# Kernel tuning notes

Hardware: AMD Instinct MI355X
Metric: run time of the kernel (lower is better)

The kernel has to match this reference:

```python
import jax, jax.numpy as jnp
import numpy as np

B, K, I, H, LAT = 128, 32, 12000, 600, 200
TAU = 0.1
EPS = 1e-12  # torch F.normalize eps


def _l2norm(x):
    return x / jnp.maximum(jnp.linalg.norm(x, axis=-1, keepdims=True), EPS)


def _l1norm(x):
    return x / jnp.maximum(jnp.sum(jnp.abs(x), axis=-1, keepdims=True), EPS)


def setup_inputs() -> dict:
    key = jax.random.key(0)
    ks = jax.random.split(key, 8)
    rating_matrix = jax.random.normal(ks[0], (B, I), dtype=jnp.float32)
    items_idx = jax.random.randint(ks[1], (B, K), 0, I)
    gram_matrix = jax.random.normal(ks[2], (I, I), dtype=jnp.float32)
    # xavier-ish scaling so tanh / exp stay in a sane range
    W1 = jax.random.normal(ks[3], (I, H), dtype=jnp.float32) * (1.0 / np.sqrt(I))
    b1 = jax.random.normal(ks[4], (H,), dtype=jnp.float32) * 0.001
    W2 = jax.random.normal(ks[5], (H, 2 * LAT), dtype=jnp.float32) * (1.0 / np.sqrt(H))
    b2 = jax.random.normal(ks[6], (2 * LAT,), dtype=jnp.float32) * 0.001
    items = jax.random.normal(ks[7], (I, LAT), dtype=jnp.float32)
    return {"rating_matrix": rating_matrix, "items_idx": items_idx,
            "gram_matrix": gram_matrix, "W1": W1, "b1": b1,
            "W2": W2, "b2": b2, "items": items}


def reference(rating_matrix, items_idx, gram_matrix, W1, b1, W2, b2, items):
    # eval-mode forward_kernel_1226 with a fixed K interacted items per user
    b0 = _l2norm(rating_matrix)                       # [B, I]
    u = (b0 > 0).astype(rating_matrix.dtype)          # binary user row [B, I]
    g = gram_matrix[items_idx]                        # gather: [B, K, I]
    x = _l2norm(_l1norm(g * u[:, None, :]))           # mask + L1 + L2 normalize
    h = jnp.tanh(jnp.einsum('bki,ih->bkh', x, W1) + b1)
    enc = jnp.einsum('bkh,ho->bko', h, W2) + b2       # [B, K, 2*LAT]
    mean, logvar = jnp.split(enc, 2, axis=-1)
    z = mean                                          # eval: z = mean
    out = jnp.einsum('bkd,id->bki', _l2norm(z), _l2norm(items)) / TAU
    # equal-length segmented mean-exp-log reduce over the K rows per user
    new_output = jnp.log(jnp.mean(jnp.exp(out), axis=1) + 1.0)  # [B, I]
    kl = 0.5 * jnp.mean(jnp.sum(mean ** 2 + jnp.exp(logvar) - 1.0 - logvar, axis=-1))
    return z.reshape(B * K, LAT), new_output, kl, x.reshape(B * K, I)
```

## Files before the change

kernel.cpp:

```cpp
#include <hip/hip_runtime.h>

typedef unsigned short u16;
typedef __attribute__((ext_vector_type(8))) short bf16x8;
typedef __attribute__((ext_vector_type(4))) float f32x4;

#define MFMA16x16(a, b, c) __builtin_amdgcn_mfma_f32_16x16x32_bf16((a), (b), (c), 0, 0, 0)

#define N_B 128
#define N_K 32
#define N_I 12000
#define N_H 600
#define N_HP 640
#define N_LAT 200
#define N_DP 224
#define N_2LAT 400
#define N_ROWS 4096
#define EPSF 1e-12f

#define OFF_NO 819200
#define OFF_KL 2355200
#define OFF_X  2355201

__device__ __forceinline__ u16 f2bf(float f) {
    unsigned u = __builtin_bit_cast(unsigned, f);
    return (u16)((u + 0x7fffu + ((u >> 16) & 1u)) >> 16);
}

__global__ __launch_bounds__(256) void k_w1t(const float* __restrict__ W1, u16* __restrict__ w1t) {
    __shared__ float tile[32][33];
    const int k0 = blockIdx.x * 32, n0 = blockIdx.y * 32;
    const int x = threadIdx.x, y = threadIdx.y;
#pragma unroll
    for (int r = 0; r < 4; r++) {
        int kk = y * 4 + r;
        int n = n0 + x;
        tile[kk][x] = (n < N_H) ? W1[(size_t)(k0 + kk) * N_H + n] : 0.f;
    }
    __syncthreads();
#pragma unroll
    for (int r = 0; r < 4; r++) {
        int nl = y * 4 + r;
        w1t[(size_t)(n0 + nl) * N_I + k0 + x] = f2bf(tile[x][nl]);
    }
}

__global__ __launch_bounds__(256) void k_w2t(const float* __restrict__ W2, u16* __restrict__ w2t) {
    __shared__ float tile[32][33];
    const int k0 = blockIdx.x * 32, n0 = blockIdx.y * 32;
    const int x = threadIdx.x, y = threadIdx.y;
#pragma unroll
    for (int r = 0; r < 4; r++) {
        int kk = y * 4 + r;
        int n = n0 + x;
        tile[kk][x] = ((k0 + kk) < N_H && n < N_2LAT) ? W2[(size_t)(k0 + kk) * N_2LAT + n] : 0.f;
    }
    __syncthreads();
#pragma unroll
    for (int r = 0; r < 4; r++) {
        int nl = y * 4 + r;
        if (n0 + nl < N_2LAT)
            w2t[(size_t)(n0 + nl) * N_HP + k0 + x] = f2bf(tile[x][nl]);
    }
}

__global__ __launch_bounds__(256) void k_itemn(const float* __restrict__ items, u16* __restrict__ itn) {
    const int r = blockIdx.x * 4 + (threadIdx.x >> 6);
    const int lane = threadIdx.x & 63;
    const float4* src = (const float4*)(items + (size_t)r * N_LAT);
    float4 v = make_float4(0.f, 0.f, 0.f, 0.f);
    if (lane < 50) v = src[lane];
    float sq = v.x * v.x + v.y * v.y + v.z * v.z + v.w * v.w;
#pragma unroll
    for (int m = 1; m < 64; m <<= 1) sq += __shfl_xor(sq, m);
    const float inv = 1.f / fmaxf(sqrtf(sq), EPSF);
    u16* dst = itn + (size_t)r * N_DP;
    if (lane < 50) {
        ushort4 pk;
        pk.x = f2bf(v.x * inv); pk.y = f2bf(v.y * inv);
        pk.z = f2bf(v.z * inv); pk.w = f2bf(v.w * inv);
        *(ushort4*)(dst + lane * 4) = pk;
    } else if (lane < 56) {
        ushort4 pk; pk.x = 0; pk.y = 0; pk.z = 0; pk.w = 0;
        *(ushort4*)(dst + lane * 4) = pk;
    }
}

__global__ __launch_bounds__(256) void k_xnorm(const float* __restrict__ rating, const int* __restrict__ idx,
                                               const float* __restrict__ gram, float* __restrict__ x_out,
                                               u16* __restrict__ xb) {
    const int row = blockIdx.x;
    const int b = row >> 5;
    const int gi = idx[row];
    const float4* grow = (const float4*)(gram + (size_t)gi * N_I);
    const float4* urow = (const float4*)(rating + (size_t)b * N_I);
    float sa = 0.f, sq = 0.f;
    for (int i = threadIdx.x; i < N_I / 4; i += 256) {
        float4 g = grow[i], u = urow[i];
        float m0 = u.x > 0.f ? g.x : 0.f;
        float m1 = u.y > 0.f ? g.y : 0.f;
        float m2 = u.z > 0.f ? g.z : 0.f;
        float m3 = u.w > 0.f ? g.w : 0.f;
        sa += fabsf(m0) + fabsf(m1) + fabsf(m2) + fabsf(m3);
        sq += m0 * m0 + m1 * m1 + m2 * m2 + m3 * m3;
    }
    __shared__ float red[8];
#pragma unroll
    for (int m = 1; m < 64; m <<= 1) { sa += __shfl_xor(sa, m); sq += __shfl_xor(sq, m); }
    const int w = threadIdx.x >> 6;
    if ((threadIdx.x & 63) == 0) { red[w] = sa; red[4 + w] = sq; }
    __syncthreads();
    sa = red[0] + red[1] + red[2] + red[3];
    sq = red[4] + red[5] + red[6] + red[7];
    const float s1 = fmaxf(sa, EPSF);
    const float s2 = fmaxf(sqrtf(sq) / s1, EPSF);
    const float scale = 1.f / (s1 * s2);
    float* xo = x_out + (size_t)row * N_I;
    u16* xbo = xb + (size_t)row * N_I;
    for (int i = threadIdx.x; i < N_I / 4; i += 256) {
        float4 g = grow[i], u = urow[i];
        float m0 = (u.x > 0.f ? g.x : 0.f) * scale;
        float m1 = (u.y > 0.f ? g.y : 0.f) * scale;
        float m2 = (u.z > 0.f ? g.z : 0.f) * scale;
        float m3 = (u.w > 0.f ? g.w : 0.f) * scale;
        xo[i * 4 + 0] = m0; xo[i * 4 + 1] = m1; xo[i * 4 + 2] = m2; xo[i * 4 + 3] = m3;
        ushort4 pk;
        pk.x = f2bf(m0); pk.y = f2bf(m1); pk.z = f2bf(m2); pk.w = f2bf(m3);
        *(ushort4*)(xbo + i * 4) = pk;
    }
}

__global__ __launch_bounds__(256) void k_gemm1(const u16* __restrict__ xb, const u16* __restrict__ w1t,
                                               const float* __restrict__ b1, u16* __restrict__ hbuf) {
    __shared__ u16 Als[128 * 40];
    __shared__ u16 Bls[128 * 40];
    const int m0 = blockIdx.x * 128;
    const int n0 = blockIdx.y * 128;
    const int t = threadIdx.x;
    const int lane = t & 63, w = t >> 6;
    const int wr = (w >> 1) * 64, wc = (w & 1) * 64;
    const int q = lane >> 4, l15 = lane & 15;

    const int rA0 = t >> 2, cA = t & 3;
    const int rA1 = rA0 + 64;
    const size_t xg0 = (size_t)(m0 + rA0) * N_I + cA * 8;
    const size_t xg1 = (size_t)(m0 + rA1) * N_I + cA * 8;
    const size_t wg0 = (size_t)(n0 + rA0) * N_I + cA * 8;
    const size_t wg1 = (size_t)(n0 + rA1) * N_I + cA * 8;
    const int ls0 = rA0 * 40 + cA * 8;
    const int ls1 = rA1 * 40 + cA * 8;

    f32x4 acc[4][4];
#pragma unroll
    for (int i = 0; i < 4; i++)
#pragma unroll
        for (int j = 0; j < 4; j++) acc[i][j] = (f32x4){0.f, 0.f, 0.f, 0.f};

    for (int k0 = 0; k0 < N_I; k0 += 32) {
        uint4 a0 = *(const uint4*)(xb + xg0 + k0);
        uint4 a1 = *(const uint4*)(xb + xg1 + k0);
        uint4 g0 = *(const uint4*)(w1t + wg0 + k0);
        uint4 g1 = *(const uint4*)(w1t + wg1 + k0);
        __syncthreads();
        *(uint4*)(Als + ls0) = a0;
        *(uint4*)(Als + ls1) = a1;
        *(uint4*)(Bls + ls0) = g0;
        *(uint4*)(Bls + ls1) = g1;
        __syncthreads();
        bf16x8 af[4], bf[4];
#pragma unroll
        for (int f = 0; f < 4; f++) af[f] = *(const bf16x8*)(Als + (wr + f * 16 + l15) * 40 + q * 8);
#pragma unroll
        for (int f = 0; f < 4; f++) bf[f] = *(const bf16x8*)(Bls + (wc + f * 16 + l15) * 40 + q * 8);
#pragma unroll
        for (int fm = 0; fm < 4; fm++)
#pragma unroll
            for (int fn = 0; fn < 4; fn++)
                acc[fm][fn] = MFMA16x16(af[fm], bf[fn], acc[fm][fn]);
    }
#pragma unroll
    for (int fm = 0; fm < 4; fm++) {
        const int rowb = m0 + wr + fm * 16 + q * 4;
#pragma unroll
        for (int fn = 0; fn < 4; fn++) {
            const int col = n0 + wc + fn * 16 + l15;
            const float bias = (col < N_H) ? b1[col] : 0.f;
#pragma unroll
            for (int r = 0; r < 4; r++) {
                float e = acc[fm][fn][r] + bias;
                hbuf[(size_t)(rowb + r) * N_HP + col] = f2bf(tanhf(e));
            }
        }
    }
}

__global__ __launch_bounds__(64) void k_gemm2(const u16* __restrict__ hbuf, const u16* __restrict__ w2t,
                                              const float* __restrict__ b2, float* __restrict__ z_out,
                                              float* __restrict__ kl_out, u16* __restrict__ znb) {
    const int m0 = blockIdx.x * 16;
    const int lane = threadIdx.x;
    const int q = lane >> 4, l15 = lane & 15;
    f32x4 acc[25];
#pragma unroll
    for (int f = 0; f < 25; f++) acc[f] = (f32x4){0.f, 0.f, 0.f, 0.f};
    for (int s = 0; s < N_HP / 32; s++) {
        bf16x8 a = *(const bf16x8*)(hbuf + (size_t)(m0 + l15) * N_HP + s * 32 + q * 8);
#pragma unroll
        for (int f = 0; f < 25; f++) {
            bf16x8 bb = *(const bf16x8*)(w2t + (size_t)(f * 16 + l15) * N_HP + s * 32 + q * 8);
            acc[f] = MFMA16x16(a, bb, acc[f]);
        }
    }
    float sumsq[4] = {0.f, 0.f, 0.f, 0.f}, kls[4] = {0.f, 0.f, 0.f, 0.f};
#pragma unroll
    for (int f = 0; f < 25; f++) {
        const int n = f * 16 + l15;
        const float bias = b2[n];
#pragma unroll
        for (int r = 0; r < 4; r++) {
            float e = acc[f][r] + bias;
            if (n < N_LAT) {
                sumsq[r] += e * e;
                kls[r] += e * e;
                z_out[(size_t)(m0 + q * 4 + r) * N_LAT + n] = e;
            } else {
                kls[r] += __expf(e) - 1.f - e;
            }
        }
    }
#pragma unroll
    for (int r = 0; r < 4; r++)
#pragma unroll
        for (int m = 1; m < 16; m <<= 1) {
            sumsq[r] += __shfl_xor(sumsq[r], m);
            kls[r] += __shfl_xor(kls[r], m);
        }
    float inv[4];
#pragma unroll
    for (int r = 0; r < 4; r++) inv[r] = 1.f / fmaxf(sqrtf(sumsq[r]), EPSF);
#pragma unroll
    for (int f = 0; f < 25; f++) {
        const int n = f * 16 + l15;
        const float bias = b2[n];
#pragma unroll
        for (int r = 0; r < 4; r++) {
            const int row = m0 + q * 4 + r;
            float e = acc[f][r] + bias;
            if (n < N_LAT) znb[(size_t)row * N_DP + n] = f2bf(e * inv[r]);
            else if (n < N_DP) znb[(size_t)row * N_DP + n] = 0;
        }
    }
    if (l15 == 0) {
        float s = (kls[0] + kls[1] + kls[2] + kls[3]) * (0.5f / (float)N_ROWS);
        atomicAdd(kl_out, s);
    }
}

__global__ __launch_bounds__(256) void k_outred(const u16* __restrict__ znb, const u16* __restrict__ itn,
                                                float* __restrict__ no_out) {
    __shared__ u16 zls[32 * N_DP];
    const int b = blockIdx.x;
    const int t = threadIdx.x;
    for (int i = t; i < (32 * N_DP) / 8; i += 256)
        ((uint4*)zls)[i] = ((const uint4*)(znb + (size_t)b * 32 * N_DP))[i];
    __syncthreads();
    const int lane = t & 63, w = t >> 6;
    const int q = lane >> 4, l15 = lane & 15;
    bf16x8 af[2][7];
#pragma unroll
    for (int hh = 0; hh < 2; hh++)
#pragma unroll
        for (int s = 0; s < 7; s++)
            af[hh][s] = *(const bf16x8*)(zls + (hh * 16 + l15) * N_DP + s * 32 + q * 8);
    for (int tt = blockIdx.y * 4 + w; tt < 750; tt += 128) {
        const int i0 = tt * 16;
        bf16x8 bfr[7];
#pragma unroll
        for (int s = 0; s < 7; s++)
            bfr[s] = *(const bf16x8*)(itn + (size_t)(i0 + l15) * N_DP + s * 32 + q * 8);
        f32x4 a0 = (f32x4){0.f, 0.f, 0.f, 0.f}, a1 = (f32x4){0.f, 0.f, 0.f, 0.f};
#pragma unroll
        for (int s = 0; s < 7; s++) {
            a0 = MFMA16x16(af[0][s], bfr[s], a0);
            a1 = MFMA16x16(af[1][s], bfr[s], a1);
        }
        float se = 0.f;
#pragma unroll
        for (int r = 0; r < 4; r++) se += __expf(a0[r] * 10.f) + __expf(a1[r] * 10.f);
        se += __shfl_xor(se, 16);
        se += __shfl_xor(se, 32);
        if (lane < 16)
            no_out[(size_t)b * N_I + i0 + lane] = __logf(se * (1.f / 32.f) + 1.f);
    }
}

extern "C" void kernel_launch(void* const* d_in, const int* in_sizes, int n_in,
                              void* d_out, int out_size, void* d_ws, size_t ws_size,
                              hipStream_t stream) {
    const float* rating = (const float*)d_in[0];
    const int* idx = (const int*)d_in[1];
    const float* gram = (const float*)d_in[2];
    const float* W1 = (const float*)d_in[3];
    const float* b1 = (const float*)d_in[4];
    const float* W2 = (const float*)d_in[5];
    const float* b2 = (const float*)d_in[6];
    const float* items = (const float*)d_in[7];

    float* out = (float*)d_out;
    float* z_out = out;
    float* no_out = out + OFF_NO;
    float* kl_out = out + OFF_KL;
    float* x_out = out + OFF_X;

    char* ws = (char*)d_ws;
    u16* xb   = (u16*)(ws);
    u16* w1t  = (u16*)(ws + 98304000);
    u16* w2t  = (u16*)(ws + 113664000);
    u16* hbuf = (u16*)(ws + 114176000);
    u16* znb  = (u16*)(ws + 119418880);
    u16* itn  = (u16*)(ws + 121253888);

    hipMemsetAsync(kl_out, 0, 4, stream);
    k_w1t<<<dim3(N_I / 32, N_HP / 32), dim3(32, 8), 0, stream>>>(W1, w1t);
    k_w2t<<<dim3(N_HP / 32, 13), dim3(32, 8), 0, stream>>>(W2, w2t);
    k_itemn<<<N_I / 4, 256, 0, stream>>>(items, itn);
    k_xnorm<<<N_ROWS, 256, 0, stream>>>(rating, idx, gram, x_out, xb);
    k_gemm1<<<dim3(N_ROWS / 128, N_HP / 128), 256, 0, stream>>>(xb, w1t, b1, hbuf);
    k_gemm2<<<N_ROWS / 16, 64, 0, stream>>>(hbuf, w2t, b2, z_out, kl_out, znb);
    k_outred<<<dim3(N_B, 32), 256, 0, stream>>>(znb, itn, no_out);
}
```

Before: 1.289 ms.

## Split-K gemm1 with async LDS loads, register-cached xnorm, two-user outred

The first GEMM is split along K into five chunks. Each chunk loads its tiles with direct global-to-LDS async loads and accumulates partial sums into a zeroed fp32 buffer using atomics. A separate kernel then adds the bias and applies an exp-based tanh. The base grid had only 32x5 blocks, and the split raises that parallelism at the cost of atomic traffic and an extra pass. k_xnorm now keeps the masked row in registers so gram is not read twice, k_outred handles two users per block so each item tile load is reused, and the workspace is reorganised so hbuf aliases xb.

```diff
diff --git a/kernel.cpp b/kernel.cpp
--- a/kernel.cpp
+++ b/kernel.cpp
@@ -16,6 +16,8 @@
 #define N_2LAT 400
 #define N_ROWS 4096
 #define EPSF 1e-12f
+#define SPLITK 5
+#define KC 2400
 
 #define OFF_NO 819200
 #define OFF_KL 2355200
@@ -24,6 +26,12 @@
 __device__ __forceinline__ u16 f2bf(float f) {
     unsigned u = __builtin_bit_cast(unsigned, f);
     return (u16)((u + 0x7fffu + ((u >> 16) & 1u)) >> 16);
+}
+
+__device__ __forceinline__ void async_ld16(const u16* g, u16* l) {
+    __builtin_amdgcn_global_load_lds(
+        (const __attribute__((address_space(1))) unsigned int*)g,
+        (__attribute__((address_space(3))) unsigned int*)l, 16, 0, 0);
 }
 
 __global__ __launch_bounds__(256) void k_w1t(const float* __restrict__ W1, u16* __restrict__ w1t) {
@@ -93,15 +101,22 @@
     const int gi = idx[row];
     const float4* grow = (const float4*)(gram + (size_t)gi * N_I);
     const float4* urow = (const float4*)(rating + (size_t)b * N_I);
+    float4 mv[12];
     float sa = 0.f, sq = 0.f;
-    for (int i = threadIdx.x; i < N_I / 4; i += 256) {
-        float4 g = grow[i], u = urow[i];
-        float m0 = u.x > 0.f ? g.x : 0.f;
-        float m1 = u.y > 0.f ? g.y : 0.f;
-        float m2 = u.z > 0.f ? g.z : 0.f;
-        float m3 = u.w > 0.f ? g.w : 0.f;
-        sa += fabsf(m0) + fabsf(m1) + fabsf(m2) + fabsf(m3);
-        sq += m0 * m0 + m1 * m1 + m2 * m2 + m3 * m3;
+#pragma unroll
+    for (int j = 0; j < 12; j++) {
+        int i = threadIdx.x + j * 256;
+        if (i < N_I / 4) {
+            float4 g = grow[i], u = urow[i];
+            float4 m;
+            m.x = u.x > 0.f ? g.x : 0.f;
+            m.y = u.y > 0.f ? g.y : 0.f;
+            m.z = u.z > 0.f ? g.z : 0.f;
+            m.w = u.w > 0.f ? g.w : 0.f;
+            mv[j] = m;
+            sa += fabsf(m.x) + fabsf(m.y) + fabsf(m.z) + fabsf(m.w);
+            sq += m.x * m.x + m.y * m.y + m.z * m.z + m.w * m.w;
+        }
     }
     __shared__ float red[8];
 #pragma unroll
@@ -116,38 +131,42 @@
     const float scale = 1.f / (s1 * s2);
     float* xo = x_out + (size_t)row * N_I;
     u16* xbo = xb + (size_t)row * N_I;
-    for (int i = threadIdx.x; i < N_I / 4; i += 256) {
-        float4 g = grow[i], u = urow[i];
-        float m0 = (u.x > 0.f ? g.x : 0.f) * scale;
-        float m1 = (u.y > 0.f ? g.y : 0.f) * scale;
-        float m2 = (u.z > 0.f ? g.z : 0.f) * scale;
-        float m3 = (u.w > 0.f ? g.w : 0.f) * scale;
-        xo[i * 4 + 0] = m0; xo[i * 4 + 1] = m1; xo[i * 4 + 2] = m2; xo[i * 4 + 3] = m3;
-        ushort4 pk;
-        pk.x = f2bf(m0); pk.y = f2bf(m1); pk.z = f2bf(m2); pk.w = f2bf(m3);
-        *(ushort4*)(xbo + i * 4) = pk;
+#pragma unroll
+    for (int j = 0; j < 12; j++) {
+        int i = threadIdx.x + j * 256;
+        if (i < N_I / 4) {
+            float4 m = mv[j];
+            float m0 = m.x * scale, m1 = m.y * scale, m2 = m.z * scale, m3 = m.w * scale;
+            xo[i * 4 + 0] = m0; xo[i * 4 + 1] = m1; xo[i * 4 + 2] = m2; xo[i * 4 + 3] = m3;
+            ushort4 pk;
+            pk.x = f2bf(m0); pk.y = f2bf(m1); pk.z = f2bf(m2); pk.w = f2bf(m3);
+            *(ushort4*)(xbo + i * 4) = pk;
+        }
     }
 }
 
 __global__ __launch_bounds__(256) void k_gemm1(const u16* __restrict__ xb, const u16* __restrict__ w1t,
-                                               const float* __restrict__ b1, u16* __restrict__ hbuf) {
-    __shared__ u16 Als[128 * 40];
-    __shared__ u16 Bls[128 * 40];
+                                               float* __restrict__ accbuf) {
+    __shared__ u16 Als[128 * 32];
+    __shared__ u16 Bls[128 * 32];
     const int m0 = blockIdx.x * 128;
     const int n0 = blockIdx.y * 128;
+    const int kbase = blockIdx.z * KC;
     const int t = threadIdx.x;
     const int lane = t & 63, w = t >> 6;
     const int wr = (w >> 1) * 64, wc = (w & 1) * 64;
     const int q = lane >> 4, l15 = lane & 15;
 
-    const int rA0 = t >> 2, cA = t & 3;
-    const int rA1 = rA0 + 64;
-    const size_t xg0 = (size_t)(m0 + rA0) * N_I + cA * 8;
-    const size_t xg1 = (size_t)(m0 + rA1) * N_I + cA * 8;
-    const size_t wg0 = (size_t)(n0 + rA0) * N_I + cA * 8;
-    const size_t wg1 = (size_t)(n0 + rA1) * N_I + cA * 8;
-    const int ls0 = rA0 * 40 + cA * 8;
-    const int ls1 = rA1 * 40 + cA * 8;
+    const int r0 = (2 * w) * 16 + l15;
+    const int c0 = q * 8;
+    const u16* gA0 = xb + (size_t)(m0 + r0) * N_I + kbase + c0;
+    const u16* gA1 = gA0 + (size_t)16 * N_I;
+    const u16* gB0 = w1t + (size_t)(n0 + r0) * N_I + kbase + c0;
+    const u16* gB1 = gB0 + (size_t)16 * N_I;
+    u16* lA0 = Als + (2 * w) * 512;
+    u16* lA1 = Als + (2 * w + 1) * 512;
+    u16* lB0 = Bls + (2 * w) * 512;
+    u16* lB1 = Bls + (2 * w + 1) * 512;
 
     f32x4 acc[4][4];
 #pragma unroll
@@ -155,27 +174,26 @@
 #pragma unroll
         for (int j = 0; j < 4; j++) acc[i][j] = (f32x4){0.f, 0.f, 0.f, 0.f};
 
-    for (int k0 = 0; k0 < N_I; k0 += 32) {
-        uint4 a0 = *(const uint4*)(xb + xg0 + k0);
-        uint4 a1 = *(const uint4*)(xb + xg1 + k0);
-        uint4 g0 = *(const uint4*)(w1t + wg0 + k0);
-        uint4 g1 = *(const uint4*)(w1t + wg1 + k0);
+    for (int ks = 0; ks < KC / 32; ks++) {
+        const int koff = ks * 32;
         __syncthreads();
-        *(uint4*)(Als + ls0) = a0;
-        *(uint4*)(Als + ls1) = a1;
-        *(uint4*)(Bls + ls0) = g0;
-        *(uint4*)(Bls + ls1) = g1;
+        async_ld16(gA0 + koff, lA0);
+        async_ld16(gA1 + koff, lA1);
+        async_ld16(gB0 + koff, lB0);
+        async_ld16(gB1 + koff, lB1);
         __syncthreads();
-        bf16x8 af[4], bf[4];
-#pragma unroll
-        for (int f = 0; f < 4; f++) af[f] = *(const bf16x8*)(Als + (wr + f * 16 + l15) * 40 + q * 8);
-#pragma unroll
-        for (int f = 0; f < 4; f++) bf[f] = *(const bf16x8*)(Bls + (wc + f * 16 + l15) * 40 + q * 8);
+        bf16x8 af[4], bfr[4];
+#pragma unroll
+        for (int f = 0; f < 4; f++)
+            af[f] = *(const bf16x8*)(Als + ((wr >> 4) + f) * 512 + q * 128 + l15 * 8);
+#pragma unroll
+        for (int f = 0; f < 4; f++)
+            bfr[f] = *(const bf16x8*)(Bls + ((wc >> 4) + f) * 512 + q * 128 + l15 * 8);
 #pragma unroll
         for (int fm = 0; fm < 4; fm++)
 #pragma unroll
             for (int fn = 0; fn < 4; fn++)
-                acc[fm][fn] = MFMA16x16(af[fm], bf[fn], acc[fm][fn]);
+                acc[fm][fn] = MFMA16x16(af[fm], bfr[fn], acc[fm][fn]);
     }
 #pragma unroll
     for (int fm = 0; fm < 4; fm++) {
@@ -183,14 +201,21 @@
 #pragma unroll
         for (int fn = 0; fn < 4; fn++) {
             const int col = n0 + wc + fn * 16 + l15;
-            const float bias = (col < N_H) ? b1[col] : 0.f;
-#pragma unroll
-            for (int r = 0; r < 4; r++) {
-                float e = acc[fm][fn][r] + bias;
-                hbuf[(size_t)(rowb + r) * N_HP + col] = f2bf(tanhf(e));
-            }
-        }
-    }
+            float* dst = accbuf + (size_t)rowb * N_HP + col;
+#pragma unroll
+            for (int r = 0; r < 4; r++)
+                atomicAdd(dst + (size_t)r * N_HP, acc[fm][fn][r]);
+        }
+    }
+}
+
+__global__ __launch_bounds__(256) void k_tanh(const float* __restrict__ accbuf, const float* __restrict__ b1,
+                                              u16* __restrict__ hbuf) {
+    const int i = blockIdx.x * 256 + threadIdx.x;
+    const int col = i % N_HP;
+    float e = accbuf[i] + (col < N_H ? b1[col] : 0.f);
+    float ex = __expf(2.f * e);
+    hbuf[i] = f2bf((ex - 1.f) / (ex + 1.f));
 }
 
 __global__ __launch_bounds__(64) void k_gemm2(const u16* __restrict__ hbuf, const u16* __restrict__ w2t,
@@ -257,39 +282,46 @@
 
 __global__ __launch_bounds__(256) void k_outred(const u16* __restrict__ znb, const u16* __restrict__ itn,
                                                 float* __restrict__ no_out) {
-    __shared__ u16 zls[32 * N_DP];
-    const int b = blockIdx.x;
+    __shared__ u16 zls[64 * N_DP];
+    const int b0 = blockIdx.x * 2;
     const int t = threadIdx.x;
-    for (int i = t; i < (32 * N_DP) / 8; i += 256)
-        ((uint4*)zls)[i] = ((const uint4*)(znb + (size_t)b * 32 * N_DP))[i];
+    for (int i = t; i < (64 * N_DP) / 8; i += 256)
+        ((uint4*)zls)[i] = ((const uint4*)(znb + (size_t)b0 * 32 * N_DP))[i];
     __syncthreads();
     const int lane = t & 63, w = t >> 6;
     const int q = lane >> 4, l15 = lane & 15;
-    bf16x8 af[2][7];
-#pragma unroll
-    for (int hh = 0; hh < 2; hh++)
+    bf16x8 af[4][7];
+#pragma unroll
+    for (int u2 = 0; u2 < 4; u2++)
 #pragma unroll
         for (int s = 0; s < 7; s++)
-            af[hh][s] = *(const bf16x8*)(zls + (hh * 16 + l15) * N_DP + s * 32 + q * 8);
+            af[u2][s] = *(const bf16x8*)(zls + (u2 * 16 + l15) * N_DP + s * 32 + q * 8);
     for (int tt = blockIdx.y * 4 + w; tt < 750; tt += 128) {
         const int i0 = tt * 16;
         bf16x8 bfr[7];
 #pragma unroll
         for (int s = 0; s < 7; s++)
             bfr[s] = *(const bf16x8*)(itn + (size_t)(i0 + l15) * N_DP + s * 32 + q * 8);
-        f32x4 a0 = (f32x4){0.f, 0.f, 0.f, 0.f}, a1 = (f32x4){0.f, 0.f, 0.f, 0.f};
-#pragma unroll
-        for (int s = 0; s < 7; s++) {
-            a0 = MFMA16x16(af[0][s], bfr[s], a0);
-            a1 = MFMA16x16(af[1][s], bfr[s], a1);
-        }
-        float se = 0.f;
-#pragma unroll
-        for (int r = 0; r < 4; r++) se += __expf(a0[r] * 10.f) + __expf(a1[r] * 10.f);
-        se += __shfl_xor(se, 16);
-        se += __shfl_xor(se, 32);
-        if (lane < 16)
-            no_out[(size_t)b * N_I + i0 + lane] = __logf(se * (1.f / 32.f) + 1.f);
+        f32x4 a[4];
+#pragma unroll
+        for (int u2 = 0; u2 < 4; u2++) a[u2] = (f32x4){0.f, 0.f, 0.f, 0.f};
+#pragma unroll
+        for (int s = 0; s < 7; s++)
+#pragma unroll
+            for (int u2 = 0; u2 < 4; u2++)
+                a[u2] = MFMA16x16(af[u2][s], bfr[s], a[u2]);
+        float se0 = 0.f, se1 = 0.f;
+#pragma unroll
+        for (int r = 0; r < 4; r++) {
+            se0 += __expf(a[0][r] * 10.f) + __expf(a[1][r] * 10.f);
+            se1 += __expf(a[2][r] * 10.f) + __expf(a[3][r] * 10.f);
+        }
+        se0 += __shfl_xor(se0, 16); se0 += __shfl_xor(se0, 32);
+        se1 += __shfl_xor(se1, 16); se1 += __shfl_xor(se1, 32);
+        if (lane < 16) {
+            no_out[(size_t)b0 * N_I + i0 + lane] = __logf(se0 * (1.f / 32.f) + 1.f);
+            no_out[(size_t)(b0 + 1) * N_I + i0 + lane] = __logf(se1 * (1.f / 32.f) + 1.f);
+        }
     }
 }
 
@@ -312,19 +344,22 @@
     float* x_out = out + OFF_X;
 
     char* ws = (char*)d_ws;
-    u16* xb   = (u16*)(ws);
-    u16* w1t  = (u16*)(ws + 98304000);
-    u16* w2t  = (u16*)(ws + 113664000);
-    u16* hbuf = (u16*)(ws + 114176000);
-    u16* znb  = (u16*)(ws + 119418880);
-    u16* itn  = (u16*)(ws + 121253888);
+    u16* xb = (u16*)ws;
+    u16* hbuf = (u16*)ws;
+    u16* znb = (u16*)(ws + 5242880);
+    u16* itn = (u16*)(ws + 7077888);
+    u16* w2t = (u16*)(ws + 12453888);
+    u16* w1t = (u16*)(ws + 98304000);
+    float* accbuf = (float*)(ws + 113664000);
 
     hipMemsetAsync(kl_out, 0, 4, stream);
+    hipMemsetAsync(accbuf, 0, (size_t)N_ROWS * N_HP * 4, stream);
     k_w1t<<<dim3(N_I / 32, N_HP / 32), dim3(32, 8), 0, stream>>>(W1, w1t);
+    k_xnorm<<<N_ROWS, 256, 0, stream>>>(rating, idx, gram, x_out, xb);
+    k_gemm1<<<dim3(N_ROWS / 128, N_HP / 128, SPLITK), 256, 0, stream>>>(xb, w1t, accbuf);
+    k_tanh<<<(N_ROWS * N_HP) / 256, 256, 0, stream>>>(accbuf, b1, hbuf);
     k_w2t<<<dim3(N_HP / 32, 13), dim3(32, 8), 0, stream>>>(W2, w2t);
     k_itemn<<<N_I / 4, 256, 0, stream>>>(items, itn);
-    k_xnorm<<<N_ROWS, 256, 0, stream>>>(rating, idx, gram, x_out, xb);
-    k_gemm1<<<dim3(N_ROWS / 128, N_HP / 128), 256, 0, stream>>>(xb, w1t, b1, hbuf);
     k_gemm2<<<N_ROWS / 16, 64, 0, stream>>>(hbuf, w2t, b2, z_out, kl_out, znb);
-    k_outred<<<dim3(N_B, 32), 256, 0, stream>>>(znb, itn, no_out);
-}
+    k_outred<<<dim3(N_B / 2, 32), 256, 0, stream>>>(znb, itn, no_out);
+}
```

Measured after the change: 1.080 ms. 1.19x faster.
